# Kernel tuning notes

Measured on AMD Instinct MI355X. Metric: run time of the kernel, lower is better.

## Reference

```python
import jax, jax.numpy as jnp
import numpy as np

B, SQ, SKV, D, H = 2, 2048, 2048, 1024, 16
HD = D // H  # 64
ROPE_BASE = 10000.0


def setup_inputs() -> dict:
    key = jax.random.key(0)
    ks = jax.random.split(key, 6)
    s = 1.0 / np.sqrt(D)  # keep activations well-scaled
    return {
        "x_q": jax.random.normal(ks[0], (B, SQ, D), jnp.float32),
        "x_kv": jax.random.normal(ks[1], (B, SKV, D), jnp.float32),
        "wq": jax.random.normal(ks[2], (D, D), jnp.float32) * s,
        "bq": jnp.zeros((D,), jnp.float32),
        "wk": jax.random.normal(ks[3], (D, D), jnp.float32) * s,
        "bk": jnp.zeros((D,), jnp.float32),
        "wv": jax.random.normal(ks[4], (D, D), jnp.float32) * s,
        "bv": jnp.zeros((D,), jnp.float32),
        "wo": jax.random.normal(ks[5], (D, D), jnp.float32) * s,
        "bo": jnp.zeros((D,), jnp.float32),
    }


def _rope_interleaved(x):
    # x: [B, S, H, HD]; sequential positions starting at 0 (GPT-NeoX style)
    s, hd = x.shape[1], x.shape[-1]
    dim = hd // 2
    freqs = jnp.exp(-jnp.arange(dim, dtype=x.dtype) * jnp.log(jnp.asarray(ROPE_BASE, x.dtype)) / dim)
    ang = jnp.arange(s, dtype=x.dtype)[:, None] * freqs[None, :]  # [S, dim]
    cos = jnp.cos(ang)[None, :, None, :]
    sin = jnp.sin(ang)[None, :, None, :]
    xe, xo = x[..., ::2], x[..., 1::2]
    re = xe * cos - xo * sin
    ro = xe * sin + xo * cos
    return jnp.stack([re, ro], axis=-1).reshape(x.shape)


def reference(x_q, x_kv, wq, bq, wk, bk, wv, bv, wo, bo):
    b, sq, _ = x_q.shape
    skv = x_kv.shape[1]
    q = (jnp.einsum("bsd,ed->bse", x_q, wq) + bq).reshape(b, sq, H, HD)
    k = (jnp.einsum("bsd,ed->bse", x_kv, wk) + bk).reshape(b, skv, H, HD)
    v = (jnp.einsum("bsd,ed->bse", x_kv, wv) + bv).reshape(b, skv, H, HD)
    q = _rope_interleaved(q)
    k = _rope_interleaved(k)
    scores = jnp.einsum("bqhd,bkhd->bhqk", q, k) / jnp.sqrt(jnp.asarray(HD, q.dtype))
    attn = jax.nn.softmax(scores, axis=-1)
    ctx = jnp.einsum("bhqk,bkhd->bqhd", attn, v).reshape(b, sq, D)
    return jnp.einsum("bsd,ed->bse", ctx, wo) + bo
```

## Files before the change

kernel.cpp:

```cpp
#include <hip/hip_runtime.h>
#include <cstdint>

typedef __attribute__((ext_vector_type(8))) short bf16x8;
typedef __attribute__((ext_vector_type(4))) float f32x4;
typedef __attribute__((ext_vector_type(4))) unsigned int u32x4;

#define DEV static __device__ __forceinline__

DEV unsigned short f2bf(float f) {
  unsigned int u = __builtin_bit_cast(unsigned int, f);
  u += 0x7FFFu + ((u >> 16) & 1u);
  return (unsigned short)(u >> 16);
}
#if __has_builtin(__builtin_amdgcn_cvt_pk_bf16_f32)
DEV unsigned int pkbf(float a, float b) {
  auto v = __builtin_amdgcn_cvt_pk_bf16_f32(a, b);
  return __builtin_bit_cast(unsigned int, v);
}
#else
DEV unsigned int pkbf(float a, float b) {
  return (unsigned int)f2bf(a) | ((unsigned int)f2bf(b) << 16);
}
#endif
#if __has_builtin(__builtin_amdgcn_exp2f)
#define EXP2(x) __builtin_amdgcn_exp2f(x)
#else
#define EXP2(x) exp2f(x)
#endif
DEV float bfl(unsigned int u) { return __builtin_bit_cast(float, u << 16); }
DEV float bfh(unsigned int u) { return __builtin_bit_cast(float, u & 0xFFFF0000u); }

DEV void async_copy16(const unsigned short* g, unsigned short* l) {
  __builtin_amdgcn_global_load_lds(
      (const __attribute__((address_space(1))) unsigned int*)(uintptr_t)g,
      (__attribute__((address_space(3))) unsigned int*)(uintptr_t)l,
      16, 0, 0);
}

#if __has_builtin(__builtin_amdgcn_permlane32_swap) && \
    __has_builtin(__builtin_amdgcn_permlane16_swap)
DEV void pswap(unsigned a, unsigned b, unsigned& w0, unsigned& w2, int lane) {
  (void)lane;
  auto pq = __builtin_amdgcn_permlane32_swap((int)a, (int)b, false, false);
  auto wz = __builtin_amdgcn_permlane16_swap(pq[0], pq[1], false, false);
  w0 = (unsigned)wz[0];
  w2 = (unsigned)wz[1];
}
#else
DEV void pswap(unsigned a, unsigned b, unsigned& w0, unsigned& w2, int lane) {
  int q = lane >> 4, l = lane & 15;
  int src0 = ((q & 1) << 5) + l;
  int a0 = __shfl((int)a, src0), b0 = __shfl((int)b, src0);
  int a2 = __shfl((int)a, src0 + 16), b2 = __shfl((int)b, src0 + 16);
  w0 = (unsigned)(q < 2 ? a0 : b0);
  w2 = (unsigned)(q < 2 ? a2 : b2);
}
#endif

__global__ __launch_bounds__(256) void cvt8(
    const float* __restrict__ w0, const float* __restrict__ w1,
    const float* __restrict__ w2, const float* __restrict__ w3,
    const float* __restrict__ x0, const float* __restrict__ x1,
    unsigned short* __restrict__ wsb, unsigned short* __restrict__ xb)
{
  int id = blockIdx.x * 256 + threadIdx.x;
  const float* src;
  unsigned short* dp;
  int off;
  if (id < (1 << 20)) {
    int m = id >> 18;
    off = (id & 0x3FFFF) << 2;
    src = m == 0 ? w0 : m == 1 ? w1 : m == 2 ? w2 : w3;
    dp = wsb + (((size_t)m) << 20) + off;
  } else {
    int id2 = id - (1 << 20);
    int m = id2 >> 20;
    off = (id2 & 0xFFFFF) << 2;
    src = m ? x1 : x0;
    dp = xb + (((size_t)m) << 22) + off;
  }
  float4 v = *(const float4*)(src + off);
  uint2 o;
  o.x = pkbf(v.x, v.y);
  o.y = pkbf(v.z, v.w);
  *(uint2*)dp = o;
}

__global__ __launch_bounds__(256) void gemm_qkv_bf(
    const unsigned short* __restrict__ xqb,
    const unsigned short* __restrict__ xkvb,
    const unsigned short* __restrict__ wbase,
    const float* __restrict__ bq, const float* __restrict__ bk,
    const float* __restrict__ bv,
    unsigned short* __restrict__ outq, unsigned short* __restrict__ outk,
    unsigned short* __restrict__ outvT)
{
  constexpr int K = 1024;
  __shared__ unsigned short As[2][128 * 32];
  __shared__ unsigned short Bs[2][128 * 32];
  const int id = blockIdx.x;
  const int sw_id = (id & 7) * 96 + (id >> 3);
  const int z = sw_id >> 8;
  const int r = sw_id & 255;
  const int mBase = (r >> 3) << 7, nBase = (r & 7) << 7;

  const unsigned short* X = (z == 0) ? xqb : xkvb;
  const unsigned short* Wb = wbase + (((size_t)z) << 20);
  const float* bias = (z == 0) ? bq : (z == 1) ? bk : bv;

  const int tid = threadIdx.x;
  const int wave = tid >> 6, lane = tid & 63;
  const int quad = lane >> 4, l16 = lane & 15;
  const int wm = (wave >> 1) << 6, wn = (wave & 1) << 6;

  const int L0 = tid, L1 = 256 + tid;
  const int r0 = L0 >> 2, c0 = ((L0 & 3) ^ (r0 & 3)) << 3;
  const int r1 = L1 >> 2, c1 = ((L1 & 3) ^ (r1 & 3)) << 3;

  f32x4 acc[4][4] = {};

  async_copy16(X + (size_t)(mBase + r0) * K + c0, &As[0][L0 * 8]);
  async_copy16(X + (size_t)(mBase + r1) * K + c1, &As[0][L1 * 8]);
  async_copy16(Wb + (size_t)(nBase + r0) * K + c0, &Bs[0][L0 * 8]);
  async_copy16(Wb + (size_t)(nBase + r1) * K + c1, &Bs[0][L1 * 8]);
  __syncthreads();

  const int sw = (quad ^ (l16 & 3)) << 3;
  for (int it = 0; it < 32; ++it) {
    const int cur = it & 1;
    if (it < 31) {
      const int k0 = (it + 1) * 32;
      async_copy16(X + (size_t)(mBase + r0) * K + k0 + c0, &As[cur ^ 1][L0 * 8]);
      async_copy16(X + (size_t)(mBase + r1) * K + k0 + c1, &As[cur ^ 1][L1 * 8]);
      async_copy16(Wb + (size_t)(nBase + r0) * K + k0 + c0, &Bs[cur ^ 1][L0 * 8]);
      async_copy16(Wb + (size_t)(nBase + r1) * K + k0 + c1, &Bs[cur ^ 1][L1 * 8]);
    }
    bf16x8 af[4], bff[4];
#pragma unroll
    for (int t = 0; t < 4; ++t) {
      af[t]  = *(const bf16x8*)&As[cur][(wm + t * 16 + l16) * 32 + sw];
      bff[t] = *(const bf16x8*)&Bs[cur][(wn + t * 16 + l16) * 32 + sw];
    }
#pragma unroll
    for (int mt = 0; mt < 4; ++mt)
#pragma unroll
      for (int nt = 0; nt < 4; ++nt)
        acc[mt][nt] = __builtin_amdgcn_mfma_f32_16x16x32_bf16(af[mt], bff[nt], acc[mt][nt], 0, 0, 0);
    __syncthreads();
  }

  if (z < 2) {
    unsigned short* out = z ? outk : outq;
    const float qs = z ? 1.0f : 0.18033688011112042f;
    const int sBlk = (mBase & 2047) + wm + quad * 4;
#pragma unroll
    for (int nt = 0; nt < 4; ++nt) {
      int n = nBase + wn + nt * 16 + l16;
      float bv2 = bias[n];
      int h = n >> 6, hd = n & 63;
      int i = hd >> 1;
      int parity = n & 1;
      float f = exp2f(-(float)i * 0.4152410118609203f);
      float sf, cf;
      sincosf(f, &sf, &cf);
#pragma unroll
      for (int mt = 0; mt < 4; ++mt) {
        float ang = (float)(sBlk + mt * 16) * f;
        float s, c;
        sincosf(ang, &s, &c);
#pragma unroll
        for (int j = 0; j < 4; ++j) {
          float v = acc[mt][nt][j] + bv2;
          float pv = __shfl_xor(v, 1);
          float ce = c * qs;
          float se = (parity ? s : -s) * qs;
          float outv = v * ce + pv * se;
          int m = mBase + wm + mt * 16 + quad * 4 + j;
          int b = m >> 11, sv = m & 2047;
          out[(((size_t)(b * 16 + h) * 2048 + sv) << 6) + hd] = f2bf(outv);
          float c2 = c * cf - s * sf;
          s = s * cf + c * sf;
          c = c2;
        }
      }
    }
  } else {
#pragma unroll
    for (int nt = 0; nt < 4; ++nt) {
      int n = nBase + wn + nt * 16 + l16;
      float bv2 = bias[n];
      int h = n >> 6, hd = n & 63;
#pragma unroll
      for (int mt = 0; mt < 4; ++mt) {
        int m0 = mBase + wm + mt * 16 + quad * 4;
        int b = m0 >> 11, s = m0 & 2047;
        uint2 o;
        o.x = pkbf(acc[mt][nt][0] + bv2, acc[mt][nt][1] + bv2);
        o.y = pkbf(acc[mt][nt][2] + bv2, acc[mt][nt][3] + bv2);
        *(uint2*)&outvT[(((size_t)(b * 16 + h) * 64 + hd) << 11) + s] = o;
      }
    }
  }
}

__global__ __launch_bounds__(256) void attn_v8(
    const unsigned short* __restrict__ Qg,
    const unsigned short* __restrict__ Kg,
    const unsigned short* __restrict__ VT,
    unsigned short* __restrict__ Opart,
    float* __restrict__ lbuf)
{
  __shared__ unsigned short Ks[2][64 * 64];
  __shared__ unsigned short Vs[3][64 * 64];
  const int tid = threadIdx.x, wave = tid >> 6, lane = tid & 63;
  const int quad = lane >> 4, l16 = lane & 15;
  const int bh = blockIdx.x & 31;
  const int qt = (blockIdx.x >> 5) & 15;
  const int kvs = blockIdx.x >> 9;
  const int q0 = qt * 128 + wave * 32;
  const unsigned short* Qb = Qg + ((size_t)bh << 17);
  const unsigned short* Kb = Kg + ((size_t)bh << 17);
  const unsigned short* Vb = VT + ((size_t)bh << 17);

  const int L0 = tid, L1 = 256 + tid;
  const int r0 = L0 >> 3, r1 = L1 >> 3;
  const int c0 = ((L0 & 7) ^ (r0 & 7)) << 3;
  const int c1 = ((L1 & 7) ^ (r1 & 7)) << 3;

  bf16x8 qf[2][2];
#pragma unroll
  for (int mq = 0; mq < 2; ++mq)
#pragma unroll
    for (int kd = 0; kd < 2; ++kd)
      qf[mq][kd] = *(const bf16x8*)(Qb + (size_t)(q0 + mq * 16 + l16) * 64 + kd * 32 + quad * 8);

  bf16x8 onesf;
#pragma unroll
  for (int i = 0; i < 8; ++i) onesf[i] = (short)0x3F80;

  f32x4 oacc[4][2] = {};
  f32x4 laccv[2] = {};
  bf16x8 pfp[2][2];

  const int kvbeg = kvs << 10;
  const int swz = l16 & 7;

  async_copy16(Kb + (size_t)(kvbeg + r0) * 64 + c0, &Ks[0][L0 * 8]);
  async_copy16(Kb + (size_t)(kvbeg + r1) * 64 + c1, &Ks[0][L1 * 8]);
  async_copy16(Vb + (size_t)r0 * 2048 + kvbeg + c0, &Vs[0][L0 * 8]);
  async_copy16(Vb + (size_t)r1 * 2048 + kvbeg + c1, &Vs[0][L1 * 8]);
  __syncthreads();

  for (int t = 0; t < 16; ++t) {
    const int kcur = t & 1;
    if (t < 15) {
      const int kv0 = kvbeg + (t + 1) * 64;
      unsigned short* Kn = Ks[kcur ^ 1];
      unsigned short* Vn = Vs[(t + 1) % 3];
      async_copy16(Kb + (size_t)(kv0 + r0) * 64 + c0, &Kn[L0 * 8]);
      async_copy16(Kb + (size_t)(kv0 + r1) * 64 + c1, &Kn[L1 * 8]);
      async_copy16(Vb + (size_t)r0 * 2048 + kv0 + c0, &Vn[L0 * 8]);
      async_copy16(Vb + (size_t)r1 * 2048 + kv0 + c1, &Vn[L1 * 8]);
    }

    if (t > 0) {
      const unsigned short* Vp = Vs[(t - 1) % 3];
      __builtin_amdgcn_s_setprio(1);
#pragma unroll
      for (int ks = 0; ks < 2; ++ks) {
#pragma unroll
        for (int th = 0; th < 4; ++th) {
          bf16x8 vf = *(const bf16x8*)&Vp[(th * 16 + l16) * 64 + (((ks * 4 + quad) ^ swz) << 3)];
#pragma unroll
          for (int mq = 0; mq < 2; ++mq)
            oacc[th][mq] = __builtin_amdgcn_mfma_f32_16x16x32_bf16(vf, pfp[ks][mq], oacc[th][mq], 0, 0, 0);
        }
#pragma unroll
        for (int mq = 0; mq < 2; ++mq)
          laccv[mq] = __builtin_amdgcn_mfma_f32_16x16x32_bf16(onesf, pfp[ks][mq], laccv[mq], 0, 0, 0);
      }
      __builtin_amdgcn_s_setprio(0);
    }

    const unsigned short* Kc = Ks[kcur];
    f32x4 st[4][2] = {};
    __builtin_amdgcn_s_setprio(1);
#pragma unroll
    for (int kd = 0; kd < 2; ++kd)
#pragma unroll
      for (int tk = 0; tk < 4; ++tk) {
        bf16x8 kf = *(const bf16x8*)&Kc[(tk * 16 + l16) * 64 + (((kd * 4 + quad) ^ swz) << 3)];
#pragma unroll
        for (int mq = 0; mq < 2; ++mq)
          st[tk][mq] = __builtin_amdgcn_mfma_f32_16x16x32_bf16(kf, qf[mq][kd], st[tk][mq], 0, 0, 0);
      }
    __builtin_amdgcn_s_setprio(0);

#pragma unroll
    for (int mq = 0; mq < 2; ++mq)
#pragma unroll
      for (int tk = 0; tk < 4; ++tk)
#pragma unroll
        for (int jr = 0; jr < 4; ++jr)
          st[tk][mq][jr] = EXP2(st[tk][mq][jr]);

#pragma unroll
    for (int ks = 0; ks < 2; ++ks)
#pragma unroll
      for (int mq = 0; mq < 2; ++mq) {
        u32x4 pw;
#pragma unroll
        for (int w = 0; w < 2; ++w) {
          unsigned a = pkbf(st[2 * ks][mq][2 * w], st[2 * ks][mq][2 * w + 1]);
          unsigned b = pkbf(st[2 * ks + 1][mq][2 * w], st[2 * ks + 1][mq][2 * w + 1]);
          unsigned w0, w2;
          pswap(a, b, w0, w2, lane);
          pw[w] = w0;
          pw[w + 2] = w2;
        }
        pfp[ks][mq] = __builtin_bit_cast(bf16x8, pw);
      }

    __syncthreads();
  }

  {
    const unsigned short* Vp = Vs[15 % 3];
    __builtin_amdgcn_s_setprio(1);
#pragma unroll
    for (int ks = 0; ks < 2; ++ks) {
#pragma unroll
      for (int th = 0; th < 4; ++th) {
        bf16x8 vf = *(const bf16x8*)&Vp[(th * 16 + l16) * 64 + (((ks * 4 + quad) ^ swz) << 3)];
#pragma unroll
        for (int mq = 0; mq < 2; ++mq)
          oacc[th][mq] = __builtin_amdgcn_mfma_f32_16x16x32_bf16(vf, pfp[ks][mq], oacc[th][mq], 0, 0, 0);
      }
#pragma unroll
      for (int mq = 0; mq < 2; ++mq)
        laccv[mq] = __builtin_amdgcn_mfma_f32_16x16x32_bf16(onesf, pfp[ks][mq], laccv[mq], 0, 0, 0);
    }
    __builtin_amdgcn_s_setprio(0);
  }

  const int b = bh >> 4, h = bh & 15;
  unsigned short* Od = Opart + (((size_t)kvs) << 22);
#pragma unroll
  for (int mq = 0; mq < 2; ++mq) {
    int s = q0 + mq * 16 + l16;
    if (quad == 0)
      lbuf[(kvs * 32 + bh) * 2048 + s] = laccv[mq][0];
#pragma unroll
    for (int th = 0; th < 4; ++th) {
      uint2 o;
      o.x = pkbf(oacc[th][mq][0], oacc[th][mq][1]);
      o.y = pkbf(oacc[th][mq][2], oacc[th][mq][3]);
      *(uint2*)&Od[((size_t)(b * 2048 + s) << 10) + h * 64 + th * 16 + quad * 4] = o;
    }
  }
}

__global__ __launch_bounds__(256) void combine_kernel(
    const unsigned short* __restrict__ Opart, const float* __restrict__ lbuf,
    unsigned short* __restrict__ ctx)
{
  int idx = blockIdx.x * 256 + threadIdx.x;
  int m = idx >> 9;
  int c2 = idx & 511;
  int b = m >> 11, s = m & 2047;
  int h = c2 >> 5;
  int bh = b * 16 + h;
  float la = lbuf[bh * 2048 + s];
  float lb = lbuf[(32 + bh) * 2048 + s];
  float r = 1.0f / (la + lb);
  unsigned int ua = ((const unsigned int*)Opart)[idx];
  unsigned int ub = ((const unsigned int*)Opart)[(1u << 21) + idx];
  float o0 = (bfl(ua) + bfl(ub)) * r;
  float o1 = (bfh(ua) + bfh(ub)) * r;
  ((unsigned int*)ctx)[idx] = pkbf(o0, o1);
}

__global__ __launch_bounds__(256) void gemm_o_bf(
    const unsigned short* __restrict__ X,
    const unsigned short* __restrict__ Wb,
    const float* __restrict__ bias,
    float* __restrict__ out)
{
  constexpr int K = 1024;
  __shared__ unsigned short As[2][64 * 32];
  __shared__ unsigned short Bs[2][128 * 32];
  const int id = blockIdx.x;
  const int sw_id = (id & 7) * 64 + (id >> 3);
  const int mBase = (sw_id >> 3) << 6, nBase = (sw_id & 7) << 7;

  const int tid = threadIdx.x;
  const int wave = tid >> 6, lane = tid & 63;
  const int quad = lane >> 4, l16 = lane & 15;
  const int wm = (wave >> 1) << 5, wn = (wave & 1) << 6;

  const int La = tid, ra = La >> 2, ca = ((La & 3) ^ (ra & 3)) << 3;
  const int Lb1 = 256 + tid, rb1 = Lb1 >> 2, cb1 = ((Lb1 & 3) ^ (rb1 & 3)) << 3;

  f32x4 acc[2][4] = {};

  async_copy16(X + (size_t)(mBase + ra) * K + ca, &As[0][La * 8]);
  async_copy16(Wb + (size_t)(nBase + ra) * K + ca, &Bs[0][La * 8]);
  async_copy16(Wb + (size_t)(nBase + rb1) * K + cb1, &Bs[0][Lb1 * 8]);
  __syncthreads();

  const int sw = (quad ^ (l16 & 3)) << 3;
  for (int it = 0; it < 32; ++it) {
    const int cur = it & 1;
    if (it < 31) {
      const int k0 = (it + 1) * 32;
      async_copy16(X + (size_t)(mBase + ra) * K + k0 + ca, &As[cur ^ 1][La * 8]);
      async_copy16(Wb + (size_t)(nBase + ra) * K + k0 + ca, &Bs[cur ^ 1][La * 8]);
      async_copy16(Wb + (size_t)(nBase + rb1) * K + k0 + cb1, &Bs[cur ^ 1][Lb1 * 8]);
    }
    bf16x8 af[2], bff[4];
#pragma unroll
    for (int t = 0; t < 2; ++t)
      af[t] = *(const bf16x8*)&As[cur][(wm + t * 16 + l16) * 32 + sw];
#pragma unroll
    for (int t = 0; t < 4; ++t)
      bff[t] = *(const bf16x8*)&Bs[cur][(wn + t * 16 + l16) * 32 + sw];
#pragma unroll
    for (int mt = 0; mt < 2; ++mt)
#pragma unroll
      for (int nt = 0; nt < 4; ++nt)
        acc[mt][nt] = __builtin_amdgcn_mfma_f32_16x16x32_bf16(af[mt], bff[nt], acc[mt][nt], 0, 0, 0);
    __syncthreads();
  }

#pragma unroll
  for (int nt = 0; nt < 4; ++nt) {
    int n = nBase + wn + nt * 16 + l16;
    float bv = bias[n];
#pragma unroll
    for (int mt = 0; mt < 2; ++mt) {
#pragma unroll
      for (int j = 0; j < 4; ++j) {
        int m = mBase + wm + mt * 16 + quad * 4 + j;
        out[((size_t)m << 10) + n] = acc[mt][nt][j] + bv;
      }
    }
  }
}

extern "C" void kernel_launch(void* const* d_in, const int* in_sizes, int n_in,
                              void* d_out, int out_size, void* d_ws, size_t ws_size,
                              hipStream_t stream) {
  const float* x_q  = (const float*)d_in[0];
  const float* x_kv = (const float*)d_in[1];
  const float* wq   = (const float*)d_in[2];
  const float* bq   = (const float*)d_in[3];
  const float* wk   = (const float*)d_in[4];
  const float* bk   = (const float*)d_in[5];
  const float* wv   = (const float*)d_in[6];
  const float* bv   = (const float*)d_in[7];
  const float* wo   = (const float*)d_in[8];
  const float* bo   = (const float*)d_in[9];

  unsigned short* base = (unsigned short*)d_ws;
  unsigned short* ob   = (unsigned short*)d_out;

  unsigned short* wob  = base + (3u << 20);
  unsigned short* k    = base + (4u << 20);
  unsigned short* vT   = base + (8u << 20);
  unsigned short* q    = base + (12u << 20);
  unsigned short* ctx  = q;
  float*          lbuf = (float*)d_ws;
  unsigned short* xqb  = ob;
  unsigned short* xkvb = ob + (4u << 20);
  unsigned short* Opart = ob;
  float* out = (float*)d_out;

  cvt8<<<12288, 256, 0, stream>>>(wq, wk, wv, wo, x_q, x_kv, base, ob);
  gemm_qkv_bf<<<768, 256, 0, stream>>>(xqb, xkvb, base, bq, bk, bv, q, k, vT);
  attn_v8<<<1024, 256, 0, stream>>>(q, k, vT, Opart, lbuf);
  combine_kernel<<<8192, 256, 0, stream>>>(Opart, lbuf, ctx);
  gemm_o_bf<<<512, 256, 0, stream>>>(ctx, wob, bo, out);
}
```

Before: 226.5 us.

## Triple-buffer QKV and output GEMM tiles with explicit vmcnt waits

Both projection GEMMs move from double to triple buffering in shared memory, keeping two k-tiles of async copies in flight. Each iteration waits on vmcnt for the oldest stage, issues a single barrier, then launches the load for the tile two steps ahead. The trailing __syncthreads is dropped, leaving one barrier per iteration. This aims to hide global-memory latency better, at the cost of 50% more LDS per block, which may lower occupancy. It also relies on the vmcnt counts matching the number of async copies each thread issues.

Result: no change. 226.1 us (-0.2%).

```diff
diff --git a/kernel.cpp b/kernel.cpp
--- a/kernel.cpp
+++ b/kernel.cpp
@@ -96,8 +96,8 @@
     unsigned short* __restrict__ outvT)
 {
   constexpr int K = 1024;
-  __shared__ unsigned short As[2][128 * 32];
-  __shared__ unsigned short Bs[2][128 * 32];
+  __shared__ unsigned short As[3][128 * 32];
+  __shared__ unsigned short Bs[3][128 * 32];
   const int id = blockIdx.x;
   const int sw_id = (id & 7) * 96 + (id >> 3);
   const int z = sw_id >> 8;
@@ -119,22 +119,28 @@
 
   f32x4 acc[4][4] = {};
 
-  async_copy16(X + (size_t)(mBase + r0) * K + c0, &As[0][L0 * 8]);
-  async_copy16(X + (size_t)(mBase + r1) * K + c1, &As[0][L1 * 8]);
-  async_copy16(Wb + (size_t)(nBase + r0) * K + c0, &Bs[0][L0 * 8]);
-  async_copy16(Wb + (size_t)(nBase + r1) * K + c1, &Bs[0][L1 * 8]);
-  __syncthreads();
+#define QKV_STAGE(kt, bi)                                                     \
+  do {                                                                        \
+    const int k0_ = (kt) * 32;                                                \
+    async_copy16(X + (size_t)(mBase + r0) * K + k0_ + c0, &As[bi][L0 * 8]);   \
+    async_copy16(X + (size_t)(mBase + r1) * K + k0_ + c1, &As[bi][L1 * 8]);   \
+    async_copy16(Wb + (size_t)(nBase + r0) * K + k0_ + c0, &Bs[bi][L0 * 8]);  \
+    async_copy16(Wb + (size_t)(nBase + r1) * K + k0_ + c1, &Bs[bi][L1 * 8]);  \
+  } while (0)
+
+  QKV_STAGE(0, 0);
+  QKV_STAGE(1, 1);
 
   const int sw = (quad ^ (l16 & 3)) << 3;
   for (int it = 0; it < 32; ++it) {
-    const int cur = it & 1;
-    if (it < 31) {
-      const int k0 = (it + 1) * 32;
-      async_copy16(X + (size_t)(mBase + r0) * K + k0 + c0, &As[cur ^ 1][L0 * 8]);
-      async_copy16(X + (size_t)(mBase + r1) * K + k0 + c1, &As[cur ^ 1][L1 * 8]);
-      async_copy16(Wb + (size_t)(nBase + r0) * K + k0 + c0, &Bs[cur ^ 1][L0 * 8]);
-      async_copy16(Wb + (size_t)(nBase + r1) * K + k0 + c1, &Bs[cur ^ 1][L1 * 8]);
-    }
+    if (it < 31)
+      asm volatile("s_waitcnt vmcnt(4)" ::: "memory");
+    else
+      asm volatile("s_waitcnt vmcnt(0)" ::: "memory");
+    __builtin_amdgcn_s_barrier();
+    if (it < 30)
+      QKV_STAGE(it + 2, (it + 2) % 3);
+    const int cur = it % 3;
     bf16x8 af[4], bff[4];
 #pragma unroll
     for (int t = 0; t < 4; ++t) {
@@ -146,8 +152,8 @@
 #pragma unroll
       for (int nt = 0; nt < 4; ++nt)
         acc[mt][nt] = __builtin_amdgcn_mfma_f32_16x16x32_bf16(af[mt], bff[nt], acc[mt][nt], 0, 0, 0);
-    __syncthreads();
-  }
+  }
+#undef QKV_STAGE
 
   if (z < 2) {
     unsigned short* out = z ? outk : outq;
@@ -387,8 +393,8 @@
     float* __restrict__ out)
 {
   constexpr int K = 1024;
-  __shared__ unsigned short As[2][64 * 32];
-  __shared__ unsigned short Bs[2][128 * 32];
+  __shared__ unsigned short As[3][64 * 32];
+  __shared__ unsigned short Bs[3][128 * 32];
   const int id = blockIdx.x;
   const int sw_id = (id & 7) * 64 + (id >> 3);
   const int mBase = (sw_id >> 3) << 6, nBase = (sw_id & 7) << 7;
@@ -403,20 +409,27 @@
 
   f32x4 acc[2][4] = {};
 
-  async_copy16(X + (size_t)(mBase + ra) * K + ca, &As[0][La * 8]);
-  async_copy16(Wb + (size_t)(nBase + ra) * K + ca, &Bs[0][La * 8]);
-  async_copy16(Wb + (size_t)(nBase + rb1) * K + cb1, &Bs[0][Lb1 * 8]);
-  __syncthreads();
+#define O_STAGE(kt, bi)                                                        \
+  do {                                                                         \
+    const int k0_ = (kt) * 32;                                                 \
+    async_copy16(X + (size_t)(mBase + ra) * K + k0_ + ca, &As[bi][La * 8]);    \
+    async_copy16(Wb + (size_t)(nBase + ra) * K + k0_ + ca, &Bs[bi][La * 8]);   \
+    async_copy16(Wb + (size_t)(nBase + rb1) * K + k0_ + cb1, &Bs[bi][Lb1 * 8]);\
+  } while (0)
+
+  O_STAGE(0, 0);
+  O_STAGE(1, 1);
 
   const int sw = (quad ^ (l16 & 3)) << 3;
   for (int it = 0; it < 32; ++it) {
-    const int cur = it & 1;
-    if (it < 31) {
-      const int k0 = (it + 1) * 32;
-      async_copy16(X + (size_t)(mBase + ra) * K + k0 + ca, &As[cur ^ 1][La * 8]);
-      async_copy16(Wb + (size_t)(nBase + ra) * K + k0 + ca, &Bs[cur ^ 1][La * 8]);
-      async_copy16(Wb + (size_t)(nBase + rb1) * K + k0 + cb1, &Bs[cur ^ 1][Lb1 * 8]);
-    }
+    if (it < 31)
+      asm volatile("s_waitcnt vmcnt(3)" ::: "memory");
+    else
+      asm volatile("s_waitcnt vmcnt(0)" ::: "memory");
+    __builtin_amdgcn_s_barrier();
+    if (it < 30)
+      O_STAGE(it + 2, (it + 2) % 3);
+    const int cur = it % 3;
     bf16x8 af[2], bff[4];
 #pragma unroll
     for (int t = 0; t < 2; ++t)
@@ -429,8 +442,8 @@
 #pragma unroll
       for (int nt = 0; nt < 4; ++nt)
         acc[mt][nt] = __builtin_amdgcn_mfma_f32_16x16x32_bf16(af[mt], bff[nt], acc[mt][nt], 0, 0, 0);
-    __syncthreads();
-  }
+  }
+#undef O_STAGE
 
 #pragma unroll
   for (int nt = 0; nt < 4; ++nt) {
```

## Fuse K and V projections sharing x_kv tiles; triple-buffer output GEMM

Applied to the files above, without the earlier changes.

The QKV projection kernel now computes K and V in the same block, so each x_kv tile loaded into shared memory feeds both weight matrices. This drops the grid from 768 to 512 blocks and cuts redundant activation loads. The cost is more accumulator registers and shared memory in the K/V blocks, plus uneven work between Q blocks and K/V blocks. The output GEMM moves to a three-stage async pipeline with explicit vmcnt waits and one barrier per iteration, aimed at hiding load latency.

Result: slower. 239.6 us (+5.8%).

```diff
diff --git a/kernel.cpp b/kernel.cpp
--- a/kernel.cpp
+++ b/kernel.cpp
@@ -97,16 +97,16 @@
 {
   constexpr int K = 1024;
   __shared__ unsigned short As[2][128 * 32];
-  __shared__ unsigned short Bs[2][128 * 32];
+  __shared__ unsigned short B0s[2][128 * 32];
+  __shared__ unsigned short B1s[2][128 * 32];
+
   const int id = blockIdx.x;
-  const int sw_id = (id & 7) * 96 + (id >> 3);
-  const int z = sw_id >> 8;
+  const int xcd = id & 7, pos = id >> 3;
+  const int sw_id = (pos < 32) ? (xcd * 32 + pos)
+                               : (256 + xcd * 32 + (pos - 32));
+  const int zsel = sw_id >> 8;
   const int r = sw_id & 255;
   const int mBase = (r >> 3) << 7, nBase = (r & 7) << 7;
-
-  const unsigned short* X = (z == 0) ? xqb : xkvb;
-  const unsigned short* Wb = wbase + (((size_t)z) << 20);
-  const float* bias = (z == 0) ? bq : (z == 1) ? bk : bv;
 
   const int tid = threadIdx.x;
   const int wave = tid >> 6, lane = tid & 63;
@@ -116,47 +116,48 @@
   const int L0 = tid, L1 = 256 + tid;
   const int r0 = L0 >> 2, c0 = ((L0 & 3) ^ (r0 & 3)) << 3;
   const int r1 = L1 >> 2, c1 = ((L1 & 3) ^ (r1 & 3)) << 3;
-
-  f32x4 acc[4][4] = {};
-
-  async_copy16(X + (size_t)(mBase + r0) * K + c0, &As[0][L0 * 8]);
-  async_copy16(X + (size_t)(mBase + r1) * K + c1, &As[0][L1 * 8]);
-  async_copy16(Wb + (size_t)(nBase + r0) * K + c0, &Bs[0][L0 * 8]);
-  async_copy16(Wb + (size_t)(nBase + r1) * K + c1, &Bs[0][L1 * 8]);
-  __syncthreads();
-
   const int sw = (quad ^ (l16 & 3)) << 3;
-  for (int it = 0; it < 32; ++it) {
-    const int cur = it & 1;
-    if (it < 31) {
-      const int k0 = (it + 1) * 32;
-      async_copy16(X + (size_t)(mBase + r0) * K + k0 + c0, &As[cur ^ 1][L0 * 8]);
-      async_copy16(X + (size_t)(mBase + r1) * K + k0 + c1, &As[cur ^ 1][L1 * 8]);
-      async_copy16(Wb + (size_t)(nBase + r0) * K + k0 + c0, &Bs[cur ^ 1][L0 * 8]);
-      async_copy16(Wb + (size_t)(nBase + r1) * K + k0 + c1, &Bs[cur ^ 1][L1 * 8]);
-    }
-    bf16x8 af[4], bff[4];
-#pragma unroll
-    for (int t = 0; t < 4; ++t) {
-      af[t]  = *(const bf16x8*)&As[cur][(wm + t * 16 + l16) * 32 + sw];
-      bff[t] = *(const bf16x8*)&Bs[cur][(wn + t * 16 + l16) * 32 + sw];
-    }
-#pragma unroll
-    for (int mt = 0; mt < 4; ++mt)
-#pragma unroll
-      for (int nt = 0; nt < 4; ++nt)
-        acc[mt][nt] = __builtin_amdgcn_mfma_f32_16x16x32_bf16(af[mt], bff[nt], acc[mt][nt], 0, 0, 0);
+  const int sBlk = (mBase & 2047) + wm + quad * 4;
+
+  if (zsel == 0) {
+    const unsigned short* X = xqb;
+    const unsigned short* Wb = wbase;
+    f32x4 acc[4][4] = {};
+
+    async_copy16(X + (size_t)(mBase + r0) * K + c0, &As[0][L0 * 8]);
+    async_copy16(X + (size_t)(mBase + r1) * K + c1, &As[0][L1 * 8]);
+    async_copy16(Wb + (size_t)(nBase + r0) * K + c0, &B0s[0][L0 * 8]);
+    async_copy16(Wb + (size_t)(nBase + r1) * K + c1, &B0s[0][L1 * 8]);
     __syncthreads();
-  }
-
-  if (z < 2) {
-    unsigned short* out = z ? outk : outq;
-    const float qs = z ? 1.0f : 0.18033688011112042f;
-    const int sBlk = (mBase & 2047) + wm + quad * 4;
+
+    for (int it = 0; it < 32; ++it) {
+      const int cur = it & 1;
+      if (it < 31) {
+        const int k0 = (it + 1) * 32;
+        async_copy16(X + (size_t)(mBase + r0) * K + k0 + c0, &As[cur ^ 1][L0 * 8]);
+        async_copy16(X + (size_t)(mBase + r1) * K + k0 + c1, &As[cur ^ 1][L1 * 8]);
+        async_copy16(Wb + (size_t)(nBase + r0) * K + k0 + c0, &B0s[cur ^ 1][L0 * 8]);
+        async_copy16(Wb + (size_t)(nBase + r1) * K + k0 + c1, &B0s[cur ^ 1][L1 * 8]);
+      }
+      bf16x8 af[4], bff[4];
+#pragma unroll
+      for (int t = 0; t < 4; ++t) {
+        af[t]  = *(const bf16x8*)&As[cur][(wm + t * 16 + l16) * 32 + sw];
+        bff[t] = *(const bf16x8*)&B0s[cur][(wn + t * 16 + l16) * 32 + sw];
+      }
+#pragma unroll
+      for (int mt = 0; mt < 4; ++mt)
+#pragma unroll
+        for (int nt = 0; nt < 4; ++nt)
+          acc[mt][nt] = __builtin_amdgcn_mfma_f32_16x16x32_bf16(af[mt], bff[nt], acc[mt][nt], 0, 0, 0);
+      __syncthreads();
+    }
+
+    const float qs = 0.18033688011112042f;
 #pragma unroll
     for (int nt = 0; nt < 4; ++nt) {
       int n = nBase + wn + nt * 16 + l16;
-      float bv2 = bias[n];
+      float bv2 = bq[n];
       int h = n >> 6, hd = n & 63;
       int i = hd >> 1;
       int parity = n & 1;
@@ -177,7 +178,7 @@
           float outv = v * ce + pv * se;
           int m = mBase + wm + mt * 16 + quad * 4 + j;
           int b = m >> 11, sv = m & 2047;
-          out[(((size_t)(b * 16 + h) * 2048 + sv) << 6) + hd] = f2bf(outv);
+          outq[(((size_t)(b * 16 + h) * 2048 + sv) << 6) + hd] = f2bf(outv);
           float c2 = c * cf - s * sf;
           s = s * cf + c * sf;
           c = c2;
@@ -185,18 +186,90 @@
       }
     }
   } else {
+    const unsigned short* X = xkvb;
+    const unsigned short* Wk = wbase + (1u << 20);
+    const unsigned short* Wv = wbase + (2u << 20);
+    f32x4 accK[4][4] = {}, accV[4][4] = {};
+
+    async_copy16(X + (size_t)(mBase + r0) * K + c0, &As[0][L0 * 8]);
+    async_copy16(X + (size_t)(mBase + r1) * K + c1, &As[0][L1 * 8]);
+    async_copy16(Wk + (size_t)(nBase + r0) * K + c0, &B0s[0][L0 * 8]);
+    async_copy16(Wk + (size_t)(nBase + r1) * K + c1, &B0s[0][L1 * 8]);
+    async_copy16(Wv + (size_t)(nBase + r0) * K + c0, &B1s[0][L0 * 8]);
+    async_copy16(Wv + (size_t)(nBase + r1) * K + c1, &B1s[0][L1 * 8]);
+    __syncthreads();
+
+    for (int it = 0; it < 32; ++it) {
+      const int cur = it & 1;
+      if (it < 31) {
+        const int k0 = (it + 1) * 32;
+        async_copy16(X + (size_t)(mBase + r0) * K + k0 + c0, &As[cur ^ 1][L0 * 8]);
+        async_copy16(X + (size_t)(mBase + r1) * K + k0 + c1, &As[cur ^ 1][L1 * 8]);
+        async_copy16(Wk + (size_t)(nBase + r0) * K + k0 + c0, &B0s[cur ^ 1][L0 * 8]);
+        async_copy16(Wk + (size_t)(nBase + r1) * K + k0 + c1, &B0s[cur ^ 1][L1 * 8]);
+        async_copy16(Wv + (size_t)(nBase + r0) * K + k0 + c0, &B1s[cur ^ 1][L0 * 8]);
+        async_copy16(Wv + (size_t)(nBase + r1) * K + k0 + c1, &B1s[cur ^ 1][L1 * 8]);
+      }
+      bf16x8 af[4];
+#pragma unroll
+      for (int t = 0; t < 4; ++t)
+        af[t] = *(const bf16x8*)&As[cur][(wm + t * 16 + l16) * 32 + sw];
+#pragma unroll
+      for (int nt = 0; nt < 4; ++nt) {
+        bf16x8 bkf = *(const bf16x8*)&B0s[cur][(wn + nt * 16 + l16) * 32 + sw];
+#pragma unroll
+        for (int mt = 0; mt < 4; ++mt)
+          accK[mt][nt] = __builtin_amdgcn_mfma_f32_16x16x32_bf16(af[mt], bkf, accK[mt][nt], 0, 0, 0);
+        bf16x8 bvf = *(const bf16x8*)&B1s[cur][(wn + nt * 16 + l16) * 32 + sw];
+#pragma unroll
+        for (int mt = 0; mt < 4; ++mt)
+          accV[mt][nt] = __builtin_amdgcn_mfma_f32_16x16x32_bf16(af[mt], bvf, accV[mt][nt], 0, 0, 0);
+      }
+      __syncthreads();
+    }
+
 #pragma unroll
     for (int nt = 0; nt < 4; ++nt) {
       int n = nBase + wn + nt * 16 + l16;
-      float bv2 = bias[n];
+      float bv2 = bk[n];
+      int h = n >> 6, hd = n & 63;
+      int i = hd >> 1;
+      int parity = n & 1;
+      float f = exp2f(-(float)i * 0.4152410118609203f);
+      float sf, cf;
+      sincosf(f, &sf, &cf);
+#pragma unroll
+      for (int mt = 0; mt < 4; ++mt) {
+        float ang = (float)(sBlk + mt * 16) * f;
+        float s, c;
+        sincosf(ang, &s, &c);
+#pragma unroll
+        for (int j = 0; j < 4; ++j) {
+          float v = accK[mt][nt][j] + bv2;
+          float pv = __shfl_xor(v, 1);
+          float se = parity ? s : -s;
+          float outv = v * c + pv * se;
+          int m = mBase + wm + mt * 16 + quad * 4 + j;
+          int b = m >> 11, sv = m & 2047;
+          outk[(((size_t)(b * 16 + h) * 2048 + sv) << 6) + hd] = f2bf(outv);
+          float c2 = c * cf - s * sf;
+          s = s * cf + c * sf;
+          c = c2;
+        }
+      }
+    }
+#pragma unroll
+    for (int nt = 0; nt < 4; ++nt) {
+      int n = nBase + wn + nt * 16 + l16;
+      float bv2 = bv[n];
       int h = n >> 6, hd = n & 63;
 #pragma unroll
       for (int mt = 0; mt < 4; ++mt) {
         int m0 = mBase + wm + mt * 16 + quad * 4;
         int b = m0 >> 11, s = m0 & 2047;
         uint2 o;
-        o.x = pkbf(acc[mt][nt][0] + bv2, acc[mt][nt][1] + bv2);
-        o.y = pkbf(acc[mt][nt][2] + bv2, acc[mt][nt][3] + bv2);
+        o.x = pkbf(accV[mt][nt][0] + bv2, accV[mt][nt][1] + bv2);
+        o.y = pkbf(accV[mt][nt][2] + bv2, accV[mt][nt][3] + bv2);
         *(uint2*)&outvT[(((size_t)(b * 16 + h) * 64 + hd) << 11) + s] = o;
       }
     }
@@ -387,8 +460,8 @@
     float* __restrict__ out)
 {
   constexpr int K = 1024;
-  __shared__ unsigned short As[2][64 * 32];
-  __shared__ unsigned short Bs[2][128 * 32];
+  __shared__ unsigned short As[3][64 * 32];
+  __shared__ unsigned short Bs[3][128 * 32];
   const int id = blockIdx.x;
   const int sw_id = (id & 7) * 64 + (id >> 3);
   const int mBase = (sw_id >> 3) << 6, nBase = (sw_id & 7) << 7;
@@ -403,20 +476,27 @@
 
   f32x4 acc[2][4] = {};
 
-  async_copy16(X + (size_t)(mBase + ra) * K + ca, &As[0][La * 8]);
-  async_copy16(Wb + (size_t)(nBase + ra) * K + ca, &Bs[0][La * 8]);
-  async_copy16(Wb + (size_t)(nBase + rb1) * K + cb1, &Bs[0][Lb1 * 8]);
-  __syncthreads();
+#define O_STAGE(kt, bi)                                                        \
+  do {                                                                         \
+    const int k0_ = (kt) * 32;                                                 \
+    async_copy16(X + (size_t)(mBase + ra) * K + k0_ + ca, &As[bi][La * 8]);    \
+    async_copy16(Wb + (size_t)(nBase + ra) * K + k0_ + ca, &Bs[bi][La * 8]);   \
+    async_copy16(Wb + (size_t)(nBase + rb1) * K + k0_ + cb1, &Bs[bi][Lb1 * 8]);\
+  } while (0)
+
+  O_STAGE(0, 0);
+  O_STAGE(1, 1);
 
   const int sw = (quad ^ (l16 & 3)) << 3;
   for (int it = 0; it < 32; ++it) {
-    const int cur = it & 1;
-    if (it < 31) {
-      const int k0 = (it + 1) * 32;
-      async_copy16(X + (size_t)(mBase + ra) * K + k0 + ca, &As[cur ^ 1][La * 8]);
-      async_copy16(Wb + (size_t)(nBase + ra) * K + k0 + ca, &Bs[cur ^ 1][La * 8]);
-      async_copy16(Wb + (size_t)(nBase + rb1) * K + k0 + cb1, &Bs[cur ^ 1][Lb1 * 8]);
-    }
+    if (it < 31)
+      asm volatile("s_waitcnt vmcnt(3)" ::: "memory");
+    else
+      asm volatile("s_waitcnt vmcnt(0)" ::: "memory");
+    __builtin_amdgcn_s_barrier();
+    if (it < 30)
+      O_STAGE(it + 2, (it + 2) % 3);
+    const int cur = it % 3;
     bf16x8 af[2], bff[4];
 #pragma unroll
     for (int t = 0; t < 2; ++t)
@@ -429,8 +509,8 @@
 #pragma unroll
       for (int nt = 0; nt < 4; ++nt)
         acc[mt][nt] = __builtin_amdgcn_mfma_f32_16x16x32_bf16(af[mt], bff[nt], acc[mt][nt], 0, 0, 0);
-    __syncthreads();
-  }
+  }
+#undef O_STAGE
 
 #pragma unroll
   for (int nt = 0; nt < 4; ++nt) {
@@ -476,7 +556,7 @@
   float* out = (float*)d_out;
 
   cvt8<<<12288, 256, 0, stream>>>(wq, wk, wv, wo, x_q, x_kv, base, ob);
-  gemm_qkv_bf<<<768, 256, 0, stream>>>(xqb, xkvb, base, bq, bk, bv, q, k, vT);
+  gemm_qkv_bf<<<512, 256, 0, stream>>>(xqb, xkvb, base, bq, bk, bv, q, k, vT);
   attn_v8<<<1024, 256, 0, stream>>>(q, k, vT, Opart, lbuf);
   combine_kernel<<<8192, 256, 0, stream>>>(Opart, lbuf, ctx);
   gemm_o_bf<<<512, 256, 0, stream>>>(ctx, wob, bo, out);
```
